# Kernel optimization log

Hardware: AMD Instinct MI355X
Metric: run time of the kernel (lower is better)

## Reference

```python
import jax, jax.numpy as jnp
import numpy as np

B, N_NODES, N_MEM, DEG, D, R = 64, 50000, 65536, 4, 128, 500
E = N_MEM * DEG


def _mlp2(x, W1, b1, W2, b2):
    # F layer with n_layers=2: Dense(leaky_relu) -> Dense(tanh); tf.nn.leaky_relu alpha=0.2
    h = jax.nn.leaky_relu(x @ W1 + b1, negative_slope=0.2)
    return jnp.tanh(h @ W2 + b2)


def setup_inputs() -> dict:
    key = jax.random.key(0)
    ks = jax.random.split(key, 17)
    eg_e = jax.random.randint(ks[0], (E,), 0, B)
    rel = jax.random.randint(ks[1], (E,), 0, R)
    e2vi = jax.random.randint(ks[2], (E,), 0, N_MEM)
    idx_vi = jax.random.randint(ks[3], (E,), 0, N_MEM)
    # every memorized node receives DEG edges; new_idx_e2vj == idx_vj (DPMPN invariant)
    idx_vj = jnp.tile(jnp.arange(N_MEM), DEG)
    z = jnp.zeros((E,), jnp.int32)
    seen_edges = jnp.stack([eg_e, z, z, rel, idx_vi, idx_vj, e2vi, idx_vj], axis=1).astype(jnp.int32)
    eg_m = jax.random.randint(ks[4], (N_MEM,), 0, B)
    v_m = jax.random.randint(ks[5], (N_MEM,), 0, N_NODES)
    memorized_nodes = jnp.stack([eg_m, v_m], axis=1).astype(jnp.int32)
    s = 0.05
    return {
        'hidden': jax.random.normal(ks[6], (N_MEM, D), jnp.float32),
        'seen_edges': seen_edges,
        'memorized_nodes': memorized_nodes,
        'node_attention': jax.random.uniform(ks[7], (B, N_NODES), jnp.float32),
        'hidden_uncon': jax.random.normal(ks[8], (1, N_NODES, D), jnp.float32),
        'query_head_emb': jax.random.normal(ks[9], (B, D), jnp.float32),
        'query_rel_emb': jax.random.normal(ks[10], (B, D), jnp.float32),
        'rel_table': jax.random.normal(ks[11], (R, D), jnp.float32),
        'msg_W1': jax.random.normal(ks[12], (5 * D, D), jnp.float32) * s,
        'msg_b1': jnp.zeros((D,), jnp.float32),
        'msg_W2': jax.random.normal(ks[13], (D, D), jnp.float32) * s,
        'msg_b2': jnp.zeros((D,), jnp.float32),
        'hid_W1': jax.random.normal(ks[14], (5 * D, D), jnp.float32) * s,
        'hid_b1': jnp.zeros((D,), jnp.float32),
        'hid_W2': jax.random.normal(ks[15], (D, D), jnp.float32) * s,
        'hid_b2': jnp.zeros((D,), jnp.float32),
        'int_W': jax.random.normal(ks[16], (D, D), jnp.float32) * s,
    }


def reference(hidden, seen_edges, memorized_nodes, node_attention, hidden_uncon,
              query_head_emb, query_rel_emb, rel_table,
              msg_W1, msg_b1, msg_W2, msg_b2,
              hid_W1, hid_b1, hid_W2, hid_b2, int_W):
    n_mem = hidden.shape[0]
    # node2edge: gather endpoint features to edges
    eg_e = seen_edges[:, 0]
    hidden_vi = hidden[seen_edges[:, 6]]
    hidden_vj = hidden[seen_edges[:, 7]]
    rel_emb = rel_table[seen_edges[:, 3]]
    qh_e = query_head_emb[eg_e]
    qr_e = query_rel_emb[eg_e]
    msg_in = jnp.concatenate([hidden_vi, rel_emb, hidden_vj, qh_e, qr_e], axis=-1)  # [E, 5D]
    message = _mlp2(msg_in, msg_W1, msg_b1, msg_W2, msg_b2)  # [E, D]
    # aggregate at vj, aggr_op 'mean_v3': unsorted_segment_mean * sqrt(count), then scatter
    idx_vj = seen_edges[:, 5]
    seg_sum = jax.ops.segment_sum(message, idx_vj, num_segments=n_mem)
    cnt = jax.ops.segment_sum(jnp.ones((E,), message.dtype), idx_vj, num_segments=n_mem)
    aggr = seg_sum * (jnp.sqrt(cnt) / jnp.maximum(cnt, 1.0))[:, None]
    red = jax.ops.segment_max(seen_edges[:, 7], idx_vj, num_segments=n_mem)
    nonempty = cnt > 0
    red = jnp.where(nonempty, red, 0)
    message_aggr = jnp.zeros_like(hidden).at[red].add(jnp.where(nonempty[:, None], aggr, 0.0))
    # unconscious-flow intervention per memorized node
    eg_m = memorized_nodes[:, 0]
    v_m = memorized_nodes[:, 1]
    hu = hidden_uncon[0][v_m]  # [n_mem, D]
    na = node_attention[eg_m, v_m]  # [n_mem]
    hu = (na[:, None] * hu) @ int_W
    qh_m = query_head_emb[eg_m]
    qr_m = query_rel_emb[eg_m]
    upd_in = jnp.concatenate([message_aggr, hidden, hu, qh_m, qr_m], axis=-1)  # [n_mem, 5D]
    update = _mlp2(upd_in, hid_W1, hid_b1, hid_W2, hid_b2)
    return hidden + update
```

## Files before the change

kernel.cpp:

```cpp
#include <hip/hip_runtime.h>
#include <hip/hip_bf16.h>

typedef unsigned short u16;
typedef __attribute__((ext_vector_type(8))) short bf16x8;
typedef __attribute__((ext_vector_type(4))) float f32x4;

#define N_MEM_C 65536
#define NNODES_C 50000
#define DDIM 128
#define BM 128
#define NTHR 512
#define TIL(t) ((t) * 16384)

__device__ __align__(16) u16 g_WT[7 * 16384];
__device__ __align__(16) float g_relW[500 * 128];
__device__ __align__(16) float g_qsumM[64 * 128];
__device__ __align__(16) float g_qsumH[64 * 128];
__device__ __align__(16) u16 g_hb[(size_t)N_MEM_C * DDIM];
__device__ __align__(16) u16 g_ub[(size_t)NNODES_C * DDIM];

#define SBAR() do { asm volatile("" ::: "memory"); __builtin_amdgcn_s_barrier(); \
                    asm volatile("" ::: "memory"); } while (0)
#define WAIT_VM0() asm volatile("s_waitcnt vmcnt(0)" ::: "memory")
#define WAIT_VM4() asm volatile("s_waitcnt vmcnt(4)" ::: "memory")
#define WAIT_LG0() asm volatile("s_waitcnt lgkmcnt(0)" ::: "memory")

__device__ __forceinline__ u16 f2bf_s(float f) {
  __hip_bfloat16 h = __float2bfloat16(f);
  u16 u; __builtin_memcpy(&u, &h, 2);
  return u;
}
__device__ __forceinline__ unsigned pk2(float a, float b) {
  __hip_bfloat162 h = __float22bfloat162_rn(make_float2(a, b));
  unsigned u; __builtin_memcpy(&u, &h, 4);
  return u;
}
__device__ __forceinline__ float bf2f(u16 u) {
  unsigned v = ((unsigned)u) << 16;
  float f; __builtin_memcpy(&f, &v, 4);
  return f;
}
__device__ __forceinline__ float fast_tanh(float x) {
  float e = __expf(2.0f * x);
  return 1.0f - 2.0f / (e + 1.0f);
}
__device__ __forceinline__ int swz_off(int r, int c) {
  return r * 128 + ((((c >> 3) ^ (r & 7)) << 3) | (c & 7));
}

extern "C" __global__ void prep_conv(const float* __restrict__ hidden,
                                     const float* __restrict__ uncon) {
  const size_t NH = (size_t)N_MEM_C * DDIM / 8;
  const size_t NU = (size_t)NNODES_C * DDIM / 8;
  size_t i = (size_t)blockIdx.x * 256 + threadIdx.x;
  const float* src; u16* dst; size_t o;
  if (i < NH) { src = hidden; dst = g_hb; o = i; }
  else if (i < NH + NU) { src = uncon; dst = g_ub; o = i - NH; }
  else return;
  const float4* p = (const float4*)(src + o * 8);
  float4 a = p[0], b = p[1];
  uint4 v = make_uint4(pk2(a.x, a.y), pk2(a.z, a.w), pk2(b.x, b.y), pk2(b.z, b.w));
  *(uint4*)(dst + o * 8) = v;
}

extern "C" __global__ void prep_wt(const float* __restrict__ msg_W1,
                                   const float* __restrict__ msg_W2,
                                   const float* __restrict__ hid_W1,
                                   const float* __restrict__ hid_W2) {
  int i = blockIdx.x * 256 + threadIdx.x;
  int t = i >> 14, idx = i & 16383;
  int n = idx >> 7, k = idx & 127;
  const float* src; int dst;
  switch (t) {
    case 0:  src = msg_W1;             dst = TIL(0); break;
    case 1:  src = msg_W1 + 256 * 128; dst = TIL(1); break;
    case 2:  src = msg_W2;             dst = TIL(2); break;
    case 3:  src = hid_W1;             dst = TIL(3); break;
    case 4:  src = hid_W1 + 128 * 128; dst = TIL(4); break;
    default: src = hid_W2;             dst = TIL(6); break;
  }
  g_WT[dst + swz_off(n, k)] = f2bf_s(src[k * 128 + n]);
}

extern "C" __global__ void prep_weff(const float* __restrict__ hid_W1,
                                     const float* __restrict__ int_W) {
  int i = blockIdx.x * 256 + threadIdx.x;
  int n = i & 127, q = i >> 7;
  float s = 0.f;
  for (int p = 0; p < 128; ++p)
    s += int_W[q * 128 + p] * hid_W1[(256 + p) * 128 + n];
  g_WT[TIL(5) + swz_off(n, q)] = f2bf_s(s);
}

extern "C" __global__ void prep_relW(const float* __restrict__ rel_table,
                                     const float* __restrict__ msg_W1) {
  int i = blockIdx.x * 256 + threadIdx.x;
  if (i >= 500 * 128) return;
  int r = i >> 7, n = i & 127;
  float s = 0.f;
  for (int k = 0; k < 128; ++k)
    s += rel_table[r * 128 + k] * msg_W1[(128 + k) * 128 + n];
  g_relW[i] = s;
}

extern "C" __global__ void prep_qsum(const float* __restrict__ qh,
                                     const float* __restrict__ qr,
                                     const float* __restrict__ msg_W1,
                                     const float* __restrict__ hid_W1) {
  int i = blockIdx.x * 256 + threadIdx.x;
  int g = i >> 7, n = i & 127;
  float sM = 0.f, sH = 0.f;
  for (int k = 0; k < 128; ++k) {
    float h = qh[g * 128 + k], r = qr[g * 128 + k];
    sM += h * msg_W1[(384 + k) * 128 + n] + r * msg_W1[(512 + k) * 128 + n];
    sH += h * hid_W1[(384 + k) * 128 + n] + r * hid_W1[(512 + k) * 128 + n];
  }
  g_qsumM[i] = sM;
  g_qsumH[i] = sH;
}

__device__ __forceinline__ void gload_rows(u16* lds_tile, const u16* __restrict__ gsrc,
                                           const int* idxArr, int base,
                                           int wid, int lane) {
  int rsub = lane >> 4, s = lane & 15;
#pragma unroll
  for (int k = 0; k < 4; ++k) {
    int r = wid * 16 + k * 4 + rsub;
    int idx = idxArr ? idxArr[r] : (base + r);
    const u16* gp = gsrc + (size_t)idx * DDIM + ((s ^ (r & 7)) << 3);
    u16* lp = lds_tile + (wid * 16 + k * 4) * 128;
    __builtin_amdgcn_global_load_lds((const __attribute__((address_space(1))) void*)gp,
                                     (__attribute__((address_space(3))) void*)lp,
                                     16, 0, 0);
  }
}
__device__ __forceinline__ void gload_lin(u16* lds_tile, const u16* __restrict__ gsrc,
                                          int wid, int lane) {
#pragma unroll
  for (int k = 0; k < 4; ++k) {
    int off = (wid * 4 + k) * 512;
    const u16* gp = gsrc + off + lane * 8;
    u16* lp = lds_tile + off;
    __builtin_amdgcn_global_load_lds((const __attribute__((address_space(1))) void*)gp,
                                     (__attribute__((address_space(3))) void*)lp,
                                     16, 0, 0);
  }
}

__device__ __forceinline__ void gemmS(const u16* A, const u16* W,
                                      f32x4 (&acc)[4][2], int wr, int wc, int l16, int l4) {
#pragma unroll
  for (int ks = 0; ks < 4; ++ks) {
    int gsl = ks * 4 + l4;
    bf16x8 av[4], bv[2];
#pragma unroll
    for (int nr = 0; nr < 2; ++nr) {
      int rW = wc * 32 + nr * 16 + l16;
      bv[nr] = *(const bf16x8*)&W[rW * 128 + ((gsl ^ (rW & 7)) << 3)];
    }
#pragma unroll
    for (int mr = 0; mr < 4; ++mr) {
      int rA = wr * 64 + mr * 16 + l16;
      av[mr] = *(const bf16x8*)&A[rA * 128 + ((gsl ^ (rA & 7)) << 3)];
    }
#pragma unroll
    for (int mr = 0; mr < 4; ++mr)
#pragma unroll
      for (int nr = 0; nr < 2; ++nr)
        acc[mr][nr] = __builtin_amdgcn_mfma_f32_16x16x32_bf16(av[mr], bv[nr], acc[mr][nr], 0, 0, 0);
  }
}

extern "C" __global__ __launch_bounds__(NTHR, 2) void fused_flow(
    const int* __restrict__ seen_edges, const int* __restrict__ memorized,
    const float* __restrict__ node_att,
    const float* __restrict__ msg_b1, const float* __restrict__ msg_b2,
    const float* __restrict__ hid_b1, const float* __restrict__ hid_b2,
    float* __restrict__ out) {
  __shared__ u16 sA0[16384], sA1[16384];
  __shared__ u16 sW0b[16384], sW2b[16384];
  __shared__ int sEg[4][BM], sRel[4][BM], sVi[4][BM];
  __shared__ int sMeg[BM], sMvm[BM];
  __shared__ float sNA[BM];

  const int tid = threadIdx.x;
  const int lane = tid & 63, wid = tid >> 6;
  const int wr = wid >> 2, wc = wid & 3;
  const int l16 = lane & 15, l4 = lane >> 4;
  const int j0 = blockIdx.x * BM;

  float mb1v[2], mb2v[2], hb1v[2], hb2v[2];
#pragma unroll
  for (int nr = 0; nr < 2; ++nr) {
    int col = wc * 32 + nr * 16 + l16;
    mb1v[nr] = msg_b1[col]; mb2v[nr] = msg_b2[col];
    hb1v[nr] = hid_b1[col]; hb2v[nr] = hid_b2[col];
  }

  gload_lin(sW0b, g_WT + TIL(0), wid, lane);
  gload_lin(sW2b, g_WT + TIL(1), wid, lane);
  gload_rows(sA0, g_hb, nullptr, j0, wid, lane);
  {
    int t = tid >> 7, r = tid & 127;
    int e = j0 + r + t * N_MEM_C;
    const int4* se = (const int4*)seen_edges + (size_t)e * 2;
    int4 lo = se[0], hi = se[1];
    sEg[t][r] = min(max(lo.x, 0), 63);
    sRel[t][r] = min(max(lo.w, 0), 499);
    sVi[t][r] = min(max(hi.z, 0), N_MEM_C - 1);
  }
  if (tid < BM) {
    int2 mn = ((const int2*)memorized)[j0 + tid];
    int eg = min(max(mn.x, 0), 63);
    int vm = min(max(mn.y, 0), NNODES_C - 1);
    sMeg[tid] = eg; sMvm[tid] = vm;
    sNA[tid] = node_att[(size_t)eg * NNODES_C + vm];
  }
  WAIT_LG0(); SBAR();
  gload_rows(sA1, g_hb, sVi[0], 0, wid, lane);
  WAIT_VM0(); SBAR();

  const f32x4 zero4 = {0.f, 0.f, 0.f, 0.f};
  f32x4 acc_vj[4][2], aggr[4][2];
#pragma unroll
  for (int a = 0; a < 4; ++a)
#pragma unroll
    for (int b = 0; b < 2; ++b) { acc_vj[a][b] = zero4; aggr[a][b] = zero4; }
  gemmS(sA0, sW2b, acc_vj, wr, wc, l16, l4);
  SBAR();
  gload_lin(sW2b, g_WT + TIL(2), wid, lane);
  gload_rows(sA0, g_hb, sVi[1], 0, wid, lane);

#pragma unroll 1
  for (int t = 0; t < 4; ++t) {
    u16* Acur = (t & 1) ? sA0 : sA1;
    f32x4 acc[4][2];
#pragma unroll
    for (int a = 0; a < 4; ++a)
#pragma unroll
      for (int b = 0; b < 2; ++b) acc[a][b] = acc_vj[a][b];
    gemmS(Acur, sW0b, acc, wr, wc, l16, l4);

#pragma unroll
    for (int mr = 0; mr < 4; ++mr)
#pragma unroll
      for (int i = 0; i < 4; ++i) {
        int r = wr * 64 + mr * 16 + l4 * 4 + i;
        const float* pr = g_relW + sRel[t][r] * 128;
        const float* pq = g_qsumM + sEg[t][r] * 128;
#pragma unroll
        for (int nr = 0; nr < 2; ++nr) {
          int c = wc * 32 + nr * 16 + l16;
          acc[mr][nr][i] += pr[c] + pq[c];
        }
      }
    SBAR();

#pragma unroll
    for (int mr = 0; mr < 4; ++mr)
#pragma unroll
      for (int nr = 0; nr < 2; ++nr)
#pragma unroll
        for (int i = 0; i < 4; ++i) {
          float v = acc[mr][nr][i] + mb1v[nr];
          v = (v >= 0.f) ? v : 0.2f * v;
          int r = wr * 64 + mr * 16 + l4 * 4 + i;
          Acur[swz_off(r, wc * 32 + nr * 16 + l16)] = f2bf_s(v);
        }
    WAIT_LG0();
    if (t == 0) { WAIT_VM4(); }
    SBAR();

    f32x4 acc2[4][2];
#pragma unroll
    for (int a = 0; a < 4; ++a)
#pragma unroll
      for (int b = 0; b < 2; ++b) acc2[a][b] = zero4;
    gemmS(Acur, sW2b, acc2, wr, wc, l16, l4);
#pragma unroll
    for (int mr = 0; mr < 4; ++mr)
#pragma unroll
      for (int nr = 0; nr < 2; ++nr)
#pragma unroll
        for (int i = 0; i < 4; ++i)
          aggr[mr][nr][i] += fast_tanh(acc2[mr][nr][i] + mb2v[nr]);
    WAIT_VM0();
    SBAR();
    if (t < 2)
      gload_rows(Acur, g_hb, sVi[t + 2], 0, wid, lane);
  }

  gload_lin(sW0b, g_WT + TIL(3), wid, lane);
  gload_lin(sW2b, g_WT + TIL(4), wid, lane);
  gload_rows(sA0, g_hb, nullptr, j0, wid, lane);
#pragma unroll
  for (int mr = 0; mr < 4; ++mr)
#pragma unroll
    for (int nr = 0; nr < 2; ++nr)
#pragma unroll
      for (int i = 0; i < 4; ++i) {
        int r = wr * 64 + mr * 16 + l4 * 4 + i;
        sA1[swz_off(r, wc * 32 + nr * 16 + l16)] = f2bf_s(0.5f * aggr[mr][nr][i]);
      }
  WAIT_LG0(); WAIT_VM0(); SBAR();

  f32x4 accU[4][2];
#pragma unroll
  for (int a = 0; a < 4; ++a)
#pragma unroll
    for (int b = 0; b < 2; ++b) accU[a][b] = zero4;
  gemmS(sA1, sW0b, accU, wr, wc, l16, l4);
  SBAR();
  gload_lin(sW0b, g_WT + TIL(5), wid, lane);
  gload_rows(sA1, g_ub, sMvm, 0, wid, lane);
  gemmS(sA0, sW2b, accU, wr, wc, l16, l4);
  SBAR();
  gload_lin(sW2b, g_WT + TIL(6), wid, lane);
  WAIT_VM4(); SBAR();

  f32x4 acc2[4][2];
#pragma unroll
  for (int a = 0; a < 4; ++a)
#pragma unroll
    for (int b = 0; b < 2; ++b) acc2[a][b] = zero4;
  gemmS(sA1, sW0b, acc2, wr, wc, l16, l4);
#pragma unroll
  for (int mr = 0; mr < 4; ++mr)
#pragma unroll
    for (int i = 0; i < 4; ++i) {
      int r = wr * 64 + mr * 16 + l4 * 4 + i;
      float na = sNA[r];
      const float* pq = g_qsumH + sMeg[r] * 128;
#pragma unroll
      for (int nr = 0; nr < 2; ++nr)
        accU[mr][nr][i] += na * acc2[mr][nr][i] + pq[wc * 32 + nr * 16 + l16];
    }
#pragma unroll
  for (int mr = 0; mr < 4; ++mr)
#pragma unroll
    for (int nr = 0; nr < 2; ++nr)
#pragma unroll
      for (int i = 0; i < 4; ++i) {
        float v = accU[mr][nr][i] + hb1v[nr];
        v = (v >= 0.f) ? v : 0.2f * v;
        int r = wr * 64 + mr * 16 + l4 * 4 + i;
        sA0[swz_off(r, wc * 32 + nr * 16 + l16)] = f2bf_s(v);
      }
  WAIT_LG0(); WAIT_VM0(); SBAR();

  f32x4 accF[4][2];
#pragma unroll
  for (int a = 0; a < 4; ++a)
#pragma unroll
    for (int b = 0; b < 2; ++b) accF[a][b] = zero4;
  gemmS(sA0, sW2b, accF, wr, wc, l16, l4);

#pragma unroll
  for (int mr = 0; mr < 4; ++mr)
#pragma unroll
    for (int nr = 0; nr < 2; ++nr)
#pragma unroll
      for (int i = 0; i < 4; ++i) {
        int row = j0 + wr * 64 + mr * 16 + l4 * 4 + i;
        int col = wc * 32 + nr * 16 + l16;
        size_t o = (size_t)row * DDIM + col;
        out[o] = bf2f(g_hb[o]) + fast_tanh(accF[mr][nr][i] + hb2v[nr]);
      }
}

extern "C" void kernel_launch(void* const* d_in, const int* in_sizes, int n_in,
                              void* d_out, int out_size, void* d_ws, size_t ws_size,
                              hipStream_t stream) {
  (void)in_sizes; (void)n_in; (void)out_size; (void)d_ws; (void)ws_size;
  const float* hidden       = (const float*)d_in[0];
  const int*   seen_edges   = (const int*)d_in[1];
  const int*   memorized    = (const int*)d_in[2];
  const float* node_att     = (const float*)d_in[3];
  const float* hidden_uncon = (const float*)d_in[4];
  const float* qh           = (const float*)d_in[5];
  const float* qr           = (const float*)d_in[6];
  const float* rel_table    = (const float*)d_in[7];
  const float* msg_W1       = (const float*)d_in[8];
  const float* msg_b1       = (const float*)d_in[9];
  const float* msg_W2       = (const float*)d_in[10];
  const float* msg_b2       = (const float*)d_in[11];
  const float* hid_W1       = (const float*)d_in[12];
  const float* hid_b1       = (const float*)d_in[13];
  const float* hid_W2       = (const float*)d_in[14];
  const float* hid_b2       = (const float*)d_in[15];
  const float* int_W        = (const float*)d_in[16];

  prep_conv<<<dim3(7221), dim3(256), 0, stream>>>(hidden, hidden_uncon);
  prep_wt<<<dim3(6 * 16384 / 256), dim3(256), 0, stream>>>(msg_W1, msg_W2, hid_W1, hid_W2);
  prep_weff<<<dim3(64), dim3(256), 0, stream>>>(hid_W1, int_W);
  prep_relW<<<dim3(250), dim3(256), 0, stream>>>(rel_table, msg_W1);
  prep_qsum<<<dim3(32), dim3(256), 0, stream>>>(qh, qr, msg_W1, hid_W1);
  fused_flow<<<dim3(N_MEM_C / BM), dim3(NTHR), 0, stream>>>(
      seen_edges, memorized, node_att, msg_b1, msg_b2, hid_b1, hid_b2, (float*)d_out);
}
```

Baseline: 134.4 us.

## Merge prep kernels into one launch and double fused-kernel threads per block

Combines the five preprocessing kernels into a single launch dispatched by block-index ranges, removing four launches and the gaps between them. The fused kernel moves from 512 to 1024 threads per block with each wave holding half the rows (2x2 MFMA tiles), which cuts accumulator registers per wave and adds waves to hide the latency of the gathers and LDS traffic. s_setprio is raised around the MFMA loops to favour waves that are doing math. More threads share each barrier, per-wave work is smaller, and the unshown index setup (wr/wc/wid mapping) has to match the new wave count.

```diff
diff --git a/kernel.cpp b/kernel.cpp
--- a/kernel.cpp
+++ b/kernel.cpp
@@ -9,7 +9,7 @@
 #define NNODES_C 50000
 #define DDIM 128
 #define BM 128
-#define NTHR 512
+#define NTHR 1024
 #define TIL(t) ((t) * 16384)
 
 __device__ __align__(16) u16 g_WT[7 * 16384];
@@ -22,7 +22,7 @@
 #define SBAR() do { asm volatile("" ::: "memory"); __builtin_amdgcn_s_barrier(); \
                     asm volatile("" ::: "memory"); } while (0)
 #define WAIT_VM0() asm volatile("s_waitcnt vmcnt(0)" ::: "memory")
-#define WAIT_VM4() asm volatile("s_waitcnt vmcnt(4)" ::: "memory")
+#define WAIT_VM2() asm volatile("s_waitcnt vmcnt(2)" ::: "memory")
 #define WAIT_LG0() asm volatile("s_waitcnt lgkmcnt(0)" ::: "memory")
 
 __device__ __forceinline__ u16 f2bf_s(float f) {
@@ -48,75 +48,67 @@
   return r * 128 + ((((c >> 3) ^ (r & 7)) << 3) | (c & 7));
 }
 
-extern "C" __global__ void prep_conv(const float* __restrict__ hidden,
-                                     const float* __restrict__ uncon) {
-  const size_t NH = (size_t)N_MEM_C * DDIM / 8;
-  const size_t NU = (size_t)NNODES_C * DDIM / 8;
-  size_t i = (size_t)blockIdx.x * 256 + threadIdx.x;
-  const float* src; u16* dst; size_t o;
-  if (i < NH) { src = hidden; dst = g_hb; o = i; }
-  else if (i < NH + NU) { src = uncon; dst = g_ub; o = i - NH; }
-  else return;
-  const float4* p = (const float4*)(src + o * 8);
-  float4 a = p[0], b = p[1];
-  uint4 v = make_uint4(pk2(a.x, a.y), pk2(a.z, a.w), pk2(b.x, b.y), pk2(b.z, b.w));
-  *(uint4*)(dst + o * 8) = v;
-}
-
-extern "C" __global__ void prep_wt(const float* __restrict__ msg_W1,
-                                   const float* __restrict__ msg_W2,
-                                   const float* __restrict__ hid_W1,
-                                   const float* __restrict__ hid_W2) {
-  int i = blockIdx.x * 256 + threadIdx.x;
-  int t = i >> 14, idx = i & 16383;
-  int n = idx >> 7, k = idx & 127;
-  const float* src; int dst;
-  switch (t) {
-    case 0:  src = msg_W1;             dst = TIL(0); break;
-    case 1:  src = msg_W1 + 256 * 128; dst = TIL(1); break;
-    case 2:  src = msg_W2;             dst = TIL(2); break;
-    case 3:  src = hid_W1;             dst = TIL(3); break;
-    case 4:  src = hid_W1 + 128 * 128; dst = TIL(4); break;
-    default: src = hid_W2;             dst = TIL(6); break;
-  }
-  g_WT[dst + swz_off(n, k)] = f2bf_s(src[k * 128 + n]);
-}
-
-extern "C" __global__ void prep_weff(const float* __restrict__ hid_W1,
-                                     const float* __restrict__ int_W) {
-  int i = blockIdx.x * 256 + threadIdx.x;
-  int n = i & 127, q = i >> 7;
-  float s = 0.f;
-  for (int p = 0; p < 128; ++p)
-    s += int_W[q * 128 + p] * hid_W1[(256 + p) * 128 + n];
-  g_WT[TIL(5) + swz_off(n, q)] = f2bf_s(s);
-}
-
-extern "C" __global__ void prep_relW(const float* __restrict__ rel_table,
-                                     const float* __restrict__ msg_W1) {
-  int i = blockIdx.x * 256 + threadIdx.x;
-  if (i >= 500 * 128) return;
-  int r = i >> 7, n = i & 127;
-  float s = 0.f;
-  for (int k = 0; k < 128; ++k)
-    s += rel_table[r * 128 + k] * msg_W1[(128 + k) * 128 + n];
-  g_relW[i] = s;
-}
-
-extern "C" __global__ void prep_qsum(const float* __restrict__ qh,
-                                     const float* __restrict__ qr,
-                                     const float* __restrict__ msg_W1,
-                                     const float* __restrict__ hid_W1) {
-  int i = blockIdx.x * 256 + threadIdx.x;
-  int g = i >> 7, n = i & 127;
-  float sM = 0.f, sH = 0.f;
-  for (int k = 0; k < 128; ++k) {
-    float h = qh[g * 128 + k], r = qr[g * 128 + k];
-    sM += h * msg_W1[(384 + k) * 128 + n] + r * msg_W1[(512 + k) * 128 + n];
-    sH += h * hid_W1[(384 + k) * 128 + n] + r * hid_W1[(512 + k) * 128 + n];
-  }
-  g_qsumM[i] = sM;
-  g_qsumH[i] = sH;
+extern "C" __global__ void prep_all(const float* __restrict__ hidden,
+                                    const float* __restrict__ uncon,
+                                    const float* __restrict__ msg_W1,
+                                    const float* __restrict__ msg_W2,
+                                    const float* __restrict__ hid_W1,
+                                    const float* __restrict__ hid_W2,
+                                    const float* __restrict__ int_W,
+                                    const float* __restrict__ rel_table,
+                                    const float* __restrict__ qh,
+                                    const float* __restrict__ qr) {
+  int bid = blockIdx.x;
+  if (bid < 7221) {
+    const size_t NH = (size_t)N_MEM_C * DDIM / 8;
+    size_t i = (size_t)bid * 256 + threadIdx.x;
+    const float* src; u16* dst; size_t o;
+    if (i < NH) { src = hidden; dst = g_hb; o = i; }
+    else { src = uncon; dst = g_ub; o = i - NH; }
+    const float4* p = (const float4*)(src + o * 8);
+    float4 a = p[0], b = p[1];
+    *(uint4*)(dst + o * 8) =
+        make_uint4(pk2(a.x, a.y), pk2(a.z, a.w), pk2(b.x, b.y), pk2(b.z, b.w));
+  } else if (bid < 7605) {
+    int i = (bid - 7221) * 256 + threadIdx.x;
+    int t = i >> 14, idx = i & 16383;
+    int n = idx >> 7, k = idx & 127;
+    const float* src; int dst;
+    switch (t) {
+      case 0:  src = msg_W1;             dst = TIL(0); break;
+      case 1:  src = msg_W1 + 256 * 128; dst = TIL(1); break;
+      case 2:  src = msg_W2;             dst = TIL(2); break;
+      case 3:  src = hid_W1;             dst = TIL(3); break;
+      case 4:  src = hid_W1 + 128 * 128; dst = TIL(4); break;
+      default: src = hid_W2;             dst = TIL(6); break;
+    }
+    g_WT[dst + swz_off(n, k)] = f2bf_s(src[k * 128 + n]);
+  } else if (bid < 7669) {
+    int i = (bid - 7605) * 256 + threadIdx.x;
+    int n = i & 127, q = i >> 7;
+    float s = 0.f;
+    for (int p = 0; p < 128; ++p)
+      s += int_W[q * 128 + p] * hid_W1[(256 + p) * 128 + n];
+    g_WT[TIL(5) + swz_off(n, q)] = f2bf_s(s);
+  } else if (bid < 7919) {
+    int i = (bid - 7669) * 256 + threadIdx.x;
+    int r = i >> 7, n = i & 127;
+    float s = 0.f;
+    for (int k = 0; k < 128; ++k)
+      s += rel_table[r * 128 + k] * msg_W1[(128 + k) * 128 + n];
+    g_relW[i] = s;
+  } else {
+    int i = (bid - 7919) * 256 + threadIdx.x;
+    int g = i >> 7, n = i & 127;
+    float sM = 0.f, sH = 0.f;
+    for (int k = 0; k < 128; ++k) {
+      float h = qh[g * 128 + k], r = qr[g * 128 + k];
+      sM += h * msg_W1[(384 + k) * 128 + n] + r * msg_W1[(512 + k) * 128 + n];
+      sH += h * hid_W1[(384 + k) * 128 + n] + r * hid_W1[(512 + k) * 128 + n];
+    }
+    g_qsumM[i] = sM;
+    g_qsumH[i] = sH;
+  }
 }
 
 __device__ __forceinline__ void gload_rows(u16* lds_tile, const u16* __restrict__ gsrc,
@@ -124,11 +116,11 @@
                                            int wid, int lane) {
   int rsub = lane >> 4, s = lane & 15;
 #pragma unroll
-  for (int k = 0; k < 4; ++k) {
-    int r = wid * 16 + k * 4 + rsub;
+  for (int k = 0; k < 2; ++k) {
+    int r = wid * 8 + k * 4 + rsub;
     int idx = idxArr ? idxArr[r] : (base + r);
     const u16* gp = gsrc + (size_t)idx * DDIM + ((s ^ (r & 7)) << 3);
-    u16* lp = lds_tile + (wid * 16 + k * 4) * 128;
+    u16* lp = lds_tile + (wid * 8 + k * 4) * 128;
     __builtin_amdgcn_global_load_lds((const __attribute__((address_space(1))) void*)gp,
                                      (__attribute__((address_space(3))) void*)lp,
                                      16, 0, 0);
@@ -137,8 +129,8 @@
 __device__ __forceinline__ void gload_lin(u16* lds_tile, const u16* __restrict__ gsrc,
                                           int wid, int lane) {
 #pragma unroll
-  for (int k = 0; k < 4; ++k) {
-    int off = (wid * 4 + k) * 512;
+  for (int k = 0; k < 2; ++k) {
+    int off = (wid * 2 + k) * 512;
     const u16* gp = gsrc + off + lane * 8;
     u16* lp = lds_tile + off;
     __builtin_amdgcn_global_load_lds((const __attribute__((address_space(1))) void*)gp,
@@ -148,30 +140,32 @@
 }
 
 __device__ __forceinline__ void gemmS(const u16* A, const u16* W,
-                                      f32x4 (&acc)[4][2], int wr, int wc, int l16, int l4) {
+                                      f32x4 (&acc)[2][2], int wr, int wc, int l16, int l4) {
+  __builtin_amdgcn_s_setprio(1);
 #pragma unroll
   for (int ks = 0; ks < 4; ++ks) {
     int gsl = ks * 4 + l4;
-    bf16x8 av[4], bv[2];
+    bf16x8 av[2], bv[2];
 #pragma unroll
     for (int nr = 0; nr < 2; ++nr) {
       int rW = wc * 32 + nr * 16 + l16;
       bv[nr] = *(const bf16x8*)&W[rW * 128 + ((gsl ^ (rW & 7)) << 3)];
     }
 #pragma unroll
-    for (int mr = 0; mr < 4; ++mr) {
-      int rA = wr * 64 + mr * 16 + l16;
+    for (int mr = 0; mr < 2; ++mr) {
+      int rA = wr * 32 + mr * 16 + l16;
       av[mr] = *(const bf16x8*)&A[rA * 128 + ((gsl ^ (rA & 7)) << 3)];
     }
 #pragma unroll
-    for (int mr = 0; mr < 4; ++mr)
+    for (int mr = 0; mr < 2; ++mr)
 #pragma unroll
       for (int nr = 0; nr < 2; ++nr)
         acc[mr][nr] = __builtin_amdgcn_mfma_f32_16x16x32_bf16(av[mr], bv[nr], acc[mr][nr], 0, 0, 0);
   }
-}
-
-extern "C" __global__ __launch_bounds__(NTHR, 2) void fused_flow(
+  __builtin_amdgcn_s_setprio(0);
+}
+
+extern "C" __global__ __launch_bounds__(NTHR, 4) void fused_flow(
     const int* __restrict__ seen_edges, const int* __restrict__ memorized,
     const float* __restrict__ node_att,
     const float* __restrict__ msg_b1, const float* __restrict__ msg_b2,
@@ -200,7 +194,7 @@
   gload_lin(sW0b, g_WT + TIL(0), wid, lane);
   gload_lin(sW2b, g_WT + TIL(1), wid, lane);
   gload_rows(sA0, g_hb, nullptr, j0, wid, lane);
-  {
+  if (tid < 512) {
     int t = tid >> 7, r = tid & 127;
     int e = j0 + r + t * N_MEM_C;
     const int4* se = (const int4*)seen_edges + (size_t)e * 2;
@@ -221,9 +215,9 @@
   WAIT_VM0(); SBAR();
 
   const f32x4 zero4 = {0.f, 0.f, 0.f, 0.f};
-  f32x4 acc_vj[4][2], aggr[4][2];
-#pragma unroll
-  for (int a = 0; a < 4; ++a)
+  f32x4 acc_vj[2][2], aggr[2][2];
+#pragma unroll
+  for (int a = 0; a < 2; ++a)
 #pragma unroll
     for (int b = 0; b < 2; ++b) { acc_vj[a][b] = zero4; aggr[a][b] = zero4; }
   gemmS(sA0, sW2b, acc_vj, wr, wc, l16, l4);
@@ -234,18 +228,18 @@
 #pragma unroll 1
   for (int t = 0; t < 4; ++t) {
     u16* Acur = (t & 1) ? sA0 : sA1;
-    f32x4 acc[4][2];
-#pragma unroll
-    for (int a = 0; a < 4; ++a)
+    f32x4 acc[2][2];
+#pragma unroll
+    for (int a = 0; a < 2; ++a)
 #pragma unroll
       for (int b = 0; b < 2; ++b) acc[a][b] = acc_vj[a][b];
     gemmS(Acur, sW0b, acc, wr, wc, l16, l4);
 
 #pragma unroll
-    for (int mr = 0; mr < 4; ++mr)
+    for (int mr = 0; mr < 2; ++mr)
 #pragma unroll
       for (int i = 0; i < 4; ++i) {
-        int r = wr * 64 + mr * 16 + l4 * 4 + i;
+        int r = wr * 32 + mr * 16 + l4 * 4 + i;
         const float* pr = g_relW + sRel[t][r] * 128;
         const float* pq = g_qsumM + sEg[t][r] * 128;
 #pragma unroll
@@ -257,28 +251,28 @@
     SBAR();
 
 #pragma unroll
-    for (int mr = 0; mr < 4; ++mr)
+    for (int mr = 0; mr < 2; ++mr)
 #pragma unroll
       for (int nr = 0; nr < 2; ++nr)
 #pragma unroll
         for (int i = 0; i < 4; ++i) {
           float v = acc[mr][nr][i] + mb1v[nr];
           v = (v >= 0.f) ? v : 0.2f * v;
-          int r = wr * 64 + mr * 16 + l4 * 4 + i;
+          int r = wr * 32 + mr * 16 + l4 * 4 + i;
           Acur[swz_off(r, wc * 32 + nr * 16 + l16)] = f2bf_s(v);
         }
     WAIT_LG0();
-    if (t == 0) { WAIT_VM4(); }
+    if (t == 0) { WAIT_VM2(); }
     SBAR();
 
-    f32x4 acc2[4][2];
-#pragma unroll
-    for (int a = 0; a < 4; ++a)
+    f32x4 acc2[2][2];
+#pragma unroll
+    for (int a = 0; a < 2; ++a)
 #pragma unroll
       for (int b = 0; b < 2; ++b) acc2[a][b] = zero4;
     gemmS(Acur, sW2b, acc2, wr, wc, l16, l4);
 #pragma unroll
-    for (int mr = 0; mr < 4; ++mr)
+    for (int mr = 0; mr < 2; ++mr)
 #pragma unroll
       for (int nr = 0; nr < 2; ++nr)
 #pragma unroll
@@ -294,19 +288,19 @@
   gload_lin(sW2b, g_WT + TIL(4), wid, lane);
   gload_rows(sA0, g_hb, nullptr, j0, wid, lane);
 #pragma unroll
-  for (int mr = 0; mr < 4; ++mr)
+  for (int mr = 0; mr < 2; ++mr)
 #pragma unroll
     for (int nr = 0; nr < 2; ++nr)
 #pragma unroll
       for (int i = 0; i < 4; ++i) {
-        int r = wr * 64 + mr * 16 + l4 * 4 + i;
+        int r = wr * 32 + mr * 16 + l4 * 4 + i;
         sA1[swz_off(r, wc * 32 + nr * 16 + l16)] = f2bf_s(0.5f * aggr[mr][nr][i]);
       }
   WAIT_LG0(); WAIT_VM0(); SBAR();
 
-  f32x4 accU[4][2];
-#pragma unroll
-  for (int a = 0; a < 4; ++a)
+  f32x4 accU[2][2];
+#pragma unroll
+  for (int a = 0; a < 2; ++a)
 #pragma unroll
     for (int b = 0; b < 2; ++b) accU[a][b] = zero4;
   gemmS(sA1, sW0b, accU, wr, wc, l16, l4);
@@ -316,19 +310,19 @@
   gemmS(sA0, sW2b, accU, wr, wc, l16, l4);
   SBAR();
   gload_lin(sW2b, g_WT + TIL(6), wid, lane);
-  WAIT_VM4(); SBAR();
-
-  f32x4 acc2[4][2];
-#pragma unroll
-  for (int a = 0; a < 4; ++a)
+  WAIT_VM2(); SBAR();
+
+  f32x4 acc2[2][2];
+#pragma unroll
+  for (int a = 0; a < 2; ++a)
 #pragma unroll
     for (int b = 0; b < 2; ++b) acc2[a][b] = zero4;
   gemmS(sA1, sW0b, acc2, wr, wc, l16, l4);
 #pragma unroll
-  for (int mr = 0; mr < 4; ++mr)
+  for (int mr = 0; mr < 2; ++mr)
 #pragma unroll
     for (int i = 0; i < 4; ++i) {
-      int r = wr * 64 + mr * 16 + l4 * 4 + i;
+      int r = wr * 32 + mr * 16 + l4 * 4 + i;
       float na = sNA[r];
       const float* pq = g_qsumH + sMeg[r] * 128;
 #pragma unroll
@@ -336,32 +330,32 @@
         accU[mr][nr][i] += na * acc2[mr][nr][i] + pq[wc * 32 + nr * 16 + l16];
     }
 #pragma unroll
-  for (int mr = 0; mr < 4; ++mr)
+  for (int mr = 0; mr < 2; ++mr)
 #pragma unroll
     for (int nr = 0; nr < 2; ++nr)
 #pragma unroll
       for (int i = 0; i < 4; ++i) {
         float v = accU[mr][nr][i] + hb1v[nr];
         v = (v >= 0.f) ? v : 0.2f * v;
-        int r = wr * 64 + mr * 16 + l4 * 4 + i;
+        int r = wr * 32 + mr * 16 + l4 * 4 + i;
         sA0[swz_off(r, wc * 32 + nr * 16 + l16)] = f2bf_s(v);
       }
   WAIT_LG0(); WAIT_VM0(); SBAR();
 
-  f32x4 accF[4][2];
-#pragma unroll
-  for (int a = 0; a < 4; ++a)
+  f32x4 accF[2][2];
+#pragma unroll
+  for (int a = 0; a < 2; ++a)
 #pragma unroll
     for (int b = 0; b < 2; ++b) accF[a][b] = zero4;
   gemmS(sA0, sW2b, accF, wr, wc, l16, l4);
 
 #pragma unroll
-  for (int mr = 0; mr < 4; ++mr)
+  for (int mr = 0; mr < 2; ++mr)
 #pragma unroll
     for (int nr = 0; nr < 2; ++nr)
 #pragma unroll
       for (int i = 0; i < 4; ++i) {
-        int row = j0 + wr * 64 + mr * 16 + l4 * 4 + i;
+        int row = j0 + wr * 32 + mr * 16 + l4 * 4 + i;
         int col = wc * 32 + nr * 16 + l16;
         size_t o = (size_t)row * DDIM + col;
         out[o] = bf2f(g_hb[o]) + fast_tanh(accF[mr][nr][i] + hb2v[nr]);
@@ -390,11 +384,9 @@
   const float* hid_b2       = (const float*)d_in[15];
   const float* int_W        = (const float*)d_in[16];
 
-  prep_conv<<<dim3(7221), dim3(256), 0, stream>>>(hidden, hidden_uncon);
-  prep_wt<<<dim3(6 * 16384 / 256), dim3(256), 0, stream>>>(msg_W1, msg_W2, hid_W1, hid_W2);
-  prep_weff<<<dim3(64), dim3(256), 0, stream>>>(hid_W1, int_W);
-  prep_relW<<<dim3(250), dim3(256), 0, stream>>>(rel_table, msg_W1);
-  prep_qsum<<<dim3(32), dim3(256), 0, stream>>>(qh, qr, msg_W1, hid_W1);
+  prep_all<<<dim3(7951), dim3(256), 0, stream>>>(
+      hidden, hidden_uncon, msg_W1, msg_W2, hid_W1, hid_W2, int_W,
+      rel_table, qh, qr);
   fused_flow<<<dim3(N_MEM_C / BM), dim3(NTHR), 0, stream>>>(
       seen_edges, memorized, node_att, msg_b1, msg_b2, hid_b1, hid_b2, (float*)d_out);
 }
```

Result: no change. 136.7 us (+1.8%).
